# Optimization experiments

Measured on AMD Instinct MI355X. Metric: run time of the kernel, lower is better.

## Reference

```python
import jax, jax.numpy as jnp
import numpy as np

H = 16        # num_attention_heads
DH = 64       # attention_head_dim
D = H * DH    # model dim = 1024
FF = 4 * D    # feed-forward inner dim = 4096
SCALE = DH ** -0.5
EPS = 1e-12


def _ln(x, g, b):
    m = jnp.mean(x, axis=-1, keepdims=True)
    v = jnp.mean((x - m) ** 2, axis=-1, keepdims=True)
    return (x - m) * jax.lax.rsqrt(v + EPS) * g + b


def _attn(x, ctx, Wq, Wk, Wv, Wo, bo, mask):
    # x: [B,S,D] (already pre-normed), ctx: [B,T,D], mask: [B,T] int (1=keep) or None
    B, S, _ = x.shape
    T = ctx.shape[1]
    q = (x @ Wq).reshape(B, S, H, DH)
    k = (ctx @ Wk).reshape(B, T, H, DH)
    v = (ctx @ Wv).reshape(B, T, H, DH)
    scores = jnp.einsum('bqhd,bkhd->bhqk', q, k) * SCALE  # [B,H,S,T]
    if mask is not None:
        scores = jnp.where(mask[:, None, None, :] == 0, -jnp.inf, scores)
    probs = jax.nn.softmax(scores, axis=-1)
    out = jnp.einsum('bhqk,bkhd->bqhd', probs, v).reshape(B, S, D)
    return out @ Wo + bo


def _geglu_ff(x, Wff1, bff1, Wff2, bff2):
    y = x @ Wff1 + bff1                 # [B,S,2*FF]
    h, gate = y[..., :FF], y[..., FF:]
    # GEGLU computes exact (erf) gelu in fp32
    g = jax.nn.gelu(gate.astype(jnp.float32), approximate=False).astype(gate.dtype)
    return (h * g) @ Wff2 + bff2


def setup_inputs() -> dict:
    key = jax.random.key(0)
    ks = jax.random.split(key, 24)
    B, S, T = 4, 1024, 1024
    w = lambda k, shp: jax.random.normal(k, shp, dtype=jnp.float32) * 0.02
    inp = {
        'hidden_states': jax.random.normal(ks[0], (B, S, D), dtype=jnp.float32),
        'context': jax.random.normal(ks[1], (B, T, D), dtype=jnp.float32),
        'encoder_key_padding_mask': jnp.ones((B, T), dtype=jnp.int32),
        'g1': jnp.ones((D,), jnp.float32), 'b1': jnp.zeros((D,), jnp.float32),
        'g2': jnp.ones((D,), jnp.float32), 'b2': jnp.zeros((D,), jnp.float32),
        'g3': jnp.ones((D,), jnp.float32), 'b3': jnp.zeros((D,), jnp.float32),
        'Wq1': w(ks[2], (D, D)), 'Wk1': w(ks[3], (D, D)), 'Wv1': w(ks[4], (D, D)),
        'Wo1': w(ks[5], (D, D)), 'bo1': jnp.zeros((D,), jnp.float32),
        'Wq2': w(ks[6], (D, D)), 'Wk2': w(ks[7], (D, D)), 'Wv2': w(ks[8], (D, D)),
        'Wo2': w(ks[9], (D, D)), 'bo2': jnp.zeros((D,), jnp.float32),
        'Wff1': w(ks[10], (D, 2 * FF)), 'bff1': jnp.zeros((2 * FF,), jnp.float32),
        'Wff2': w(ks[11], (FF, D)), 'bff2': jnp.zeros((D,), jnp.float32),
    }
    return inp


def reference(hidden_states, context, encoder_key_padding_mask,
              g1, b1, g2, b2, g3, b3,
              Wq1, Wk1, Wv1, Wo1, bo1,
              Wq2, Wk2, Wv2, Wo2, bo2,
              Wff1, bff1, Wff2, bff2):
    # Self-attention (attn1): context defaults to (normed) hidden_states, no padding mask
    n1 = _ln(hidden_states, g1, b1)
    h = hidden_states + _attn(n1, n1, Wq1, Wk1, Wv1, Wo1, bo1, None)
    # Cross-attention (attn2) with encoder key padding mask
    n2 = _ln(h, g2, b2)
    h = h + _attn(n2, context, Wq2, Wk2, Wv2, Wo2, bo2, encoder_key_padding_mask)
    # GEGLU feed-forward
    h = h + _geglu_ff(_ln(h, g3, b3), Wff1, bff1, Wff2, bff2)
    return h
```

## Files before the change

### kernel.cpp

```cpp
#include <hip/hip_runtime.h>

typedef unsigned short u16;
typedef unsigned int u32;

#define B_ 4
#define S_ 1024
#define D_ 1024
#define H_ 16
#define DH_ 64
#define FF_ 4096
#define M_ 4096
#define SCALE_ 0.125f

typedef __attribute__((ext_vector_type(8))) __bf16 bf16x8;
typedef __attribute__((ext_vector_type(4))) float f32x4;

__device__ __forceinline__ f32x4 mfma16(bf16x8 a, bf16x8 b, f32x4 c) {
  return __builtin_amdgcn_mfma_f32_16x16x32_bf16(a, b, c, 0, 0, 0);
}

__device__ __forceinline__ u16 f2bf(float x) {
  union { __bf16 h; u16 u; } cv; cv.h = (__bf16)x; return cv.u;
}
__device__ __forceinline__ float bf2f(u16 u) {
  union { u32 u; float f; } cv; cv.u = ((u32)u) << 16; return cv.f;
}
__device__ __forceinline__ u32 packbf2(float a, float b) {
  union { u32 u; __bf16 h[2]; } pk;
  pk.h[0] = (__bf16)a; pk.h[1] = (__bf16)b;
  return pk.u;
}
__device__ __forceinline__ float gelu_exact(float x) {
  return 0.5f * x * (1.f + erff(x * 0.7071067811865475f));
}
__device__ __forceinline__ void gload16(const void* g, void* l) {
  __builtin_amdgcn_global_load_lds((__attribute__((address_space(1))) void*)(g),
                                   (__attribute__((address_space(3))) void*)(l),
                                   16, 0, 0);
}

template<int EPI>
__global__ __launch_bounds__(256, 2) void gemm128(
    const u16* __restrict__ A, const u16* __restrict__ BT,
    const float* __restrict__ bias, const float* __restrict__ res,
    const u16* __restrict__ aux, void* __restrict__ out,
    int M, int N, int K, int ktiles)
{
  __shared__ u16 As[2][128 * 64];
  __shared__ u16 Bs[2][128 * 64];

  const int tid = threadIdx.x;
  const int wave = tid >> 6, lane = tid & 63;
  const int wm = wave >> 1, wn = wave & 1;
  const int qi = lane & 15, g = lane >> 4;

  const int gx = N >> 7;
  const int nwg = gx * (M >> 7);
  int id = blockIdx.y * gridDim.x + blockIdx.x;
  id = (id & 7) * (nwg >> 3) + (id >> 3);
  const int m0 = (id / gx) << 7, n0 = (id % gx) << 7;

  const int NT = ktiles;
  const int kbase = blockIdx.z * ktiles * 64;

  const int r0 = tid >> 3;
  const int scol = (((tid & 7) ^ ((tid >> 3) & 7)) << 3);
  const int swb = wave << 6;

  f32x4 acc[4][4];
#pragma unroll
  for (int i = 0; i < 4; ++i)
#pragma unroll
    for (int j = 0; j < 4; ++j)
      acc[i][j] = (f32x4){0.f, 0.f, 0.f, 0.f};

#define STAGE_A(t, h, b) {                                                  \
    const int tt = (t) >= NT ? (t) - NT : (t);                              \
    _Pragma("unroll")                                                       \
    for (int i = 0; i < 2; ++i) {                                           \
      const int r = (h) * 64 + i * 32 + r0;                                 \
      gload16(A + (size_t)(m0 + r) * K + kbase + tt * 64 + scol,            \
              &As[b][(h) * 4096 + (i * 256 + swb) * 8]);                    \
    } }
#define STAGE_B(t, h, b) {                                                  \
    const int tt = (t) >= NT ? (t) - NT : (t);                              \
    _Pragma("unroll")                                                       \
    for (int i = 0; i < 2; ++i) {                                           \
      const int r = (h) * 64 + i * 32 + r0;                                 \
      gload16(BT + (size_t)(n0 + r) * K + kbase + tt * 64 + scol,           \
              &Bs[b][(h) * 4096 + (i * 256 + swb) * 8]);                    \
    } }

  bf16x8 af[4][2], bfr[4][2];

#define RD_ALL(b)                                                            \
  _Pragma("unroll") for (int mi = 0; mi < 4; ++mi)                           \
  _Pragma("unroll") for (int kk = 0; kk < 2; ++kk) {                         \
    const int row = wm * 64 + mi * 16 + qi;                                  \
    const int cb = ((kk * 64 + (g << 4)) ^ ((qi & 7) << 4));                 \
    af[mi][kk] = *(const bf16x8*)((const char*)&As[b][0] + row * 128 + cb);  \
  }                                                                          \
  _Pragma("unroll") for (int ni = 0; ni < 4; ++ni)                           \
  _Pragma("unroll") for (int kk = 0; kk < 2; ++kk) {                         \
    const int row = wn * 64 + ni * 16 + qi;                                  \
    const int cb = ((kk * 64 + (g << 4)) ^ ((qi & 7) << 4));                 \
    bfr[ni][kk] = *(const bf16x8*)((const char*)&Bs[b][0] + row * 128 + cb); \
  }

#define MFMA_ALL()                                                           \
  _Pragma("unroll") for (int mi = 0; mi < 4; ++mi)                           \
  _Pragma("unroll") for (int ni = 0; ni < 4; ++ni)                           \
  _Pragma("unroll") for (int kk = 0; kk < 2; ++kk)                           \
    acc[mi][ni] = mfma16(af[mi][kk], bfr[ni][kk], acc[mi][ni]);

#define BAR() __builtin_amdgcn_s_barrier()
#define LGKM0() { asm volatile("s_waitcnt lgkmcnt(0)" ::: "memory");         \
                  __builtin_amdgcn_sched_barrier(0); }
#define VM8() asm volatile("s_waitcnt vmcnt(8)" ::: "memory")
#define PRIO(x) __builtin_amdgcn_s_setprio(x)

  STAGE_A(0, 0, 0); STAGE_A(0, 1, 0); STAGE_B(0, 0, 0); STAGE_B(0, 1, 0);
  STAGE_A(1, 0, 1); STAGE_A(1, 1, 1); STAGE_B(1, 0, 1); STAGE_B(1, 1, 1);
  VM8();
  BAR();

  const int NI = NT >> 1;
  for (int it = 0; it < NI; ++it) {
    const int k = it * 2;
    RD_ALL(0);
    PRIO(1); MFMA_ALL(); PRIO(0);
    LGKM0();
    BAR();
    STAGE_A(k + 2, 0, 0); STAGE_A(k + 2, 1, 0);
    STAGE_B(k + 2, 0, 0); STAGE_B(k + 2, 1, 0);
    VM8();
    BAR();
    RD_ALL(1);
    PRIO(1); MFMA_ALL(); PRIO(0);
    LGKM0();
    BAR();
    STAGE_A(k + 3, 0, 1); STAGE_A(k + 3, 1, 1);
    STAGE_B(k + 3, 0, 1); STAGE_B(k + 3, 1, 1);
    VM8();
    BAR();
  }

#pragma unroll
  for (int mi = 0; mi < 4; ++mi) {
#pragma unroll
    for (int ni = 0; ni < 4; ++ni) {
#pragma unroll
      for (int r = 0; r < 4; ++r) {
        const int m = m0 + wm * 64 + mi * 16 + g * 4 + r;
        const int n = n0 + wn * 64 + ni * 16 + qi;
        float v = acc[mi][ni][r];
        if (EPI == 0 || EPI == 5) {
          const int ts = n >> 10, b = m >> 10, s = m & 1023;
          const int hh = (n >> 6) & 15, dh = n & 63;
          if (EPI == 0 && ts == 0) v *= SCALE_;
          ((u16*)out)[(size_t)ts * (B_ * H_ * S_ * DH_) +
                      (((size_t)(b * H_ + hh) * S_) + s) * DH_ + dh] = f2bf(v);
        } else if (EPI == 1) {
          const size_t idx = (size_t)m * N + n;
          ((float*)out)[idx] = res[idx] + v + bias[n];
        } else if (EPI == 2) {
          ((u16*)out)[(size_t)m * N + n] = f2bf(gelu_exact(v + bias[n]));
        } else if (EPI == 3) {
          const size_t idx = (size_t)m * N + n;
          ((u16*)out)[idx] = f2bf((v + bias[n]) * bf2f(aux[idx]));
        } else {
          const size_t idx = (size_t)blockIdx.z * ((size_t)M * N) +
                             (size_t)m * N + n;
          ((u16*)out)[idx] = f2bf(v);
        }
      }
    }
  }
#undef STAGE_A
#undef STAGE_B
#undef RD_ALL
#undef MFMA_ALL
#undef BAR
#undef LGKM0
#undef VM8
#undef PRIO
}

template<bool DOLN, int NS>
__global__ __launch_bounds__(256) void reduce_ln(
    const u16* __restrict__ p, const float* __restrict__ bias,
    const float* __restrict__ res, float* __restrict__ outf,
    const float* __restrict__ gg, const float* __restrict__ bb,
    u16* __restrict__ outn)
{
  __shared__ float red[8];
  const int row = blockIdx.x, tid = threadIdx.x;
  const size_t base = (size_t)row * 1024 + tid * 4;
  const size_t total = (size_t)M_ * 1024;
  float a0 = 0.f, a1 = 0.f, a2 = 0.f, a3 = 0.f;
#pragma unroll
  for (int s = 0; s < NS; ++s) {
    const uint2 u = *(const uint2*)&p[(size_t)s * total + base];
    a0 += bf2f((u16)(u.x & 0xffff));
    a1 += bf2f((u16)(u.x >> 16));
    a2 += bf2f((u16)(u.y & 0xffff));
    a3 += bf2f((u16)(u.y >> 16));
  }
  const float4 b4 = ((const float4*)bias)[tid];
  const float4 r4 = *(const float4*)&res[base];
  float4 o;
  o.x = r4.x + a0 + b4.x;
  o.y = r4.y + a1 + b4.y;
  o.z = r4.z + a2 + b4.z;
  o.w = r4.w + a3 + b4.w;
  *(float4*)&outf[base] = o;

  if (DOLN) {
    float s1 = o.x + o.y + o.z + o.w;
    float s2 = o.x * o.x + o.y * o.y + o.z * o.z + o.w * o.w;
#pragma unroll
    for (int m = 32; m; m >>= 1) {
      s1 += __shfl_xor(s1, m);
      s2 += __shfl_xor(s2, m);
    }
    const int wave = tid >> 6, lane = tid & 63;
    if (lane == 0) { red[wave * 2] = s1; red[wave * 2 + 1] = s2; }
    __syncthreads();
    const float St = red[0] + red[2] + red[4] + red[6];
    const float SQt = red[1] + red[3] + red[5] + red[7];
    const float mean = St * (1.f / 1024.f);
    float var = SQt * (1.f / 1024.f) - mean * mean;
    var = fmaxf(var, 0.f);
    const float rinv = rsqrtf(var + 1e-12f);
    const float4 g4 = ((const float4*)gg)[tid];
    const float4 bb4 = ((const float4*)bb)[tid];
    uint2 w;
    w.x = packbf2((o.x - mean) * rinv * g4.x + bb4.x,
                  (o.y - mean) * rinv * g4.y + bb4.y);
    w.y = packbf2((o.z - mean) * rinv * g4.z + bb4.z,
                  (o.w - mean) * rinv * g4.w + bb4.w);
    ((uint2*)(outn + (size_t)row * 1024))[tid] = w;
  }
}

template<int NS, bool QSC>
__global__ __launch_bounds__(256) void reduce_perm(
    const u16* __restrict__ p, u16* __restrict__ out, int M, int N)
{
  const size_t flat = ((size_t)blockIdx.x * 256 + threadIdx.x) * 4;
  const size_t total = (size_t)M * N;
  float a0 = 0.f, a1 = 0.f, a2 = 0.f, a3 = 0.f;
#pragma unroll
  for (int s = 0; s < NS; ++s) {
    const uint2 u = *(const uint2*)&p[(size_t)s * total + flat];
    a0 += bf2f((u16)(u.x & 0xffff));
    a1 += bf2f((u16)(u.x >> 16));
    a2 += bf2f((u16)(u.y & 0xffff));
    a3 += bf2f((u16)(u.y >> 16));
  }
  if (QSC) { a0 *= SCALE_; a1 *= SCALE_; a2 *= SCALE_; a3 *= SCALE_; }
  const int m = (int)(flat / N), nb = (int)(flat % N);
  const int ts = nb >> 10, hh = (nb >> 6) & 15, dh = nb & 63;
  const int b = m >> 10, sI = m & 1023;
  uint2 w;
  w.x = packbf2(a0, a1);
  w.y = packbf2(a2, a3);
  *(uint2*)&out[(size_t)ts * (B_ * H_ * S_ * DH_) +
                (((size_t)(b * H_ + hh) * S_) + sI) * DH_ + dh] = w;
}

template<bool MASKED>
__global__ __launch_bounds__(256, 4) void attn_kernel(
    const u16* __restrict__ Q, const u16* __restrict__ Kb,
    const u16* __restrict__ VT, const float* __restrict__ bias,
    u16* __restrict__ O, int S, int T)
{
  __shared__ u16 Ks[64 * 72];
  __shared__ u16 VTs[64 * 72];
  __shared__ u16 Ps[4][16 * 72];
  __shared__ float biasS[64];

  const int bh = blockIdx.y;
  const int b = bh >> 4, h = bh & 15;
  const int tid = threadIdx.x;
  const int wave = tid >> 6, lane = tid & 63;
  const int g = lane >> 4, qi = lane & 15;
  const int q0w = blockIdx.x * 64 + wave * 16;

  const u16* Qb = Q + (size_t)bh * S * DH_;
  const u16* Kg = Kb + (size_t)bh * T * DH_;
  const u16* Vg = VT + (size_t)bh * DH_ * T;

  bf16x8 qf[2];
  qf[0] = *(const bf16x8*)&Qb[(q0w + qi) * DH_ + g * 8];
  qf[1] = *(const bf16x8*)&Qb[(q0w + qi) * DH_ + 32 + g * 8];

  f32x4 acc[4];
#pragma unroll
  for (int i = 0; i < 4; ++i) acc[i] = (f32x4){0.f, 0.f, 0.f, 0.f};
  float l_run = 1e-30f;

  u16* Pw = &Ps[wave][0];

  for (int t0 = 0; t0 < T; t0 += 64) {
    __syncthreads();
#pragma unroll
    for (int i = 0; i < 2; ++i) {
      const int flat = i * 256 + tid;
      const int row = flat >> 3, kc = flat & 7;
      *(uint4*)&Ks[row * 72 + kc * 8] = *(const uint4*)&Kg[(size_t)(t0 + row) * DH_ + kc * 8];
      *(uint4*)&VTs[row * 72 + kc * 8] = *(const uint4*)&Vg[(size_t)row * T + t0 + kc * 8];
    }
    if (MASKED && tid < 64) biasS[tid] = bias[b * T + t0 + tid];
    __syncthreads();

    f32x4 sacc[4];
#pragma unroll
    for (int nt = 0; nt < 4; ++nt) sacc[nt] = (f32x4){0.f, 0.f, 0.f, 0.f};
#pragma unroll
    for (int kk = 0; kk < 2; ++kk) {
#pragma unroll
      for (int nt = 0; nt < 4; ++nt) {
        bf16x8 kf = *(const bf16x8*)&Ks[(nt * 16 + qi) * 72 + kk * 32 + g * 8];
        sacc[nt] = mfma16(kf, qf[kk], sacc[nt]);
      }
    }
    float p[4][4];
    float lsum = 0.f;
#pragma unroll
    for (int nt = 0; nt < 4; ++nt)
#pragma unroll
      for (int r = 0; r < 4; ++r) {
        float v = sacc[nt][r];
        if (MASKED) v += biasS[nt * 16 + g * 4 + r];
        const float e = __expf(v);
        p[nt][r] = e;
        lsum += e;
      }
    lsum += __shfl_xor(lsum, 16);
    lsum += __shfl_xor(lsum, 32);
    l_run += lsum;

#pragma unroll
    for (int nt = 0; nt < 4; ++nt) {
      uint2 w;
      w.x = packbf2(p[nt][0], p[nt][1]);
      w.y = packbf2(p[nt][2], p[nt][3]);
      *(uint2*)&Pw[qi * 72 + nt * 16 + g * 4] = w;
    }

#pragma unroll
    for (int kk = 0; kk < 2; ++kk) {
      bf16x8 pf = *(const bf16x8*)&Pw[qi * 72 + kk * 32 + g * 8];
#pragma unroll
      for (int ndh = 0; ndh < 4; ++ndh) {
        bf16x8 vf = *(const bf16x8*)&VTs[(ndh * 16 + qi) * 72 + kk * 32 + g * 8];
        acc[ndh] = mfma16(vf, pf, acc[ndh]);
      }
    }
  }

  const float inv = 1.f / l_run;
  const int qg = q0w + qi;
#pragma unroll
  for (int ndh = 0; ndh < 4; ++ndh) {
    uint2 w;
    w.x = packbf2(acc[ndh][0] * inv, acc[ndh][1] * inv);
    w.y = packbf2(acc[ndh][2] * inv, acc[ndh][3] * inv);
    *(uint2*)&O[(size_t)(b * S_ + qg) * D_ + h * DH_ + ndh * 16 + g * 4] = w;
  }
}

__global__ __launch_bounds__(256) void ln_kernel(
    const float* __restrict__ x, const float* __restrict__ gg,
    const float* __restrict__ bb, u16* __restrict__ out)
{
  __shared__ float red[8];
  const int row = blockIdx.x, tid = threadIdx.x;
  const float4 v = ((const float4*)(x + (size_t)row * D_))[tid];
  float s = v.x + v.y + v.z + v.w;
  float sq = v.x * v.x + v.y * v.y + v.z * v.z + v.w * v.w;
#pragma unroll
  for (int m = 32; m; m >>= 1) {
    s += __shfl_xor(s, m);
    sq += __shfl_xor(sq, m);
  }
  const int wave = tid >> 6, lane = tid & 63;
  if (lane == 0) { red[wave * 2] = s; red[wave * 2 + 1] = sq; }
  __syncthreads();
  const float St = red[0] + red[2] + red[4] + red[6];
  const float SQt = red[1] + red[3] + red[5] + red[7];
  const float mean = St * (1.f / 1024.f);
  float var = SQt * (1.f / 1024.f) - mean * mean;
  var = fmaxf(var, 0.f);
  const float rinv = rsqrtf(var + 1e-12f);
  const float4 g4 = ((const float4*)gg)[tid];
  const float4 b4 = ((const float4*)bb)[tid];
  uint2 o;
  o.x = packbf2((v.x - mean) * rinv * g4.x + b4.x, (v.y - mean) * rinv * g4.y + b4.y);
  o.y = packbf2((v.z - mean) * rinv * g4.z + b4.z, (v.w - mean) * rinv * g4.w + b4.w);
  ((uint2*)(out + (size_t)row * D_))[tid] = o;
}

__global__ __launch_bounds__(256) void transpose_w(
    const float* __restrict__ in, u16* __restrict__ out, int K, int N)
{
  __shared__ float tile[32][33];
  const int tx = threadIdx.x & 31, ty = threadIdx.x >> 5;
  const int k0 = blockIdx.y * 32, n0 = blockIdx.x * 32;
#pragma unroll
  for (int j = 0; j < 4; ++j)
    tile[ty + 8 * j][tx] = in[(size_t)(k0 + ty + 8 * j) * N + n0 + tx];
  __syncthreads();
#pragma unroll
  for (int j = 0; j < 4; ++j)
    out[(size_t)(n0 + ty + 8 * j) * K + k0 + tx] = f2bf(tile[tx][ty + 8 * j]);
}

__global__ __launch_bounds__(256) void transpose_v(
    const u16* __restrict__ in, u16* __restrict__ out, int T)
{
  __shared__ u16 tile[32][33];
  const int tx = threadIdx.x & 31, ty = threadIdx.x >> 5;
  const int bh = blockIdx.z;
  const int t0 = blockIdx.x * 32, d0 = blockIdx.y * 32;
  const u16* ib = in + (size_t)bh * T * DH_;
  u16* ob = out + (size_t)bh * DH_ * T;
#pragma unroll
  for (int j = 0; j < 4; ++j)
    tile[ty + 8 * j][tx] = ib[(size_t)(t0 + ty + 8 * j) * DH_ + d0 + tx];
  __syncthreads();
#pragma unroll
  for (int j = 0; j < 4; ++j)
    ob[(size_t)(d0 + ty + 8 * j) * T + t0 + tx] = tile[tx][ty + 8 * j];
}

__global__ void cvt_bf16(const float* __restrict__ in, u16* __restrict__ out, int n4)
{
  const int i = blockIdx.x * blockDim.x + threadIdx.x;
  if (i < n4) {
    const float4 v = ((const float4*)in)[i];
    uint2 o;
    o.x = packbf2(v.x, v.y);
    o.y = packbf2(v.z, v.w);
    ((uint2*)out)[i] = o;
  }
}

__global__ void mask_bias(const int* __restrict__ mask, float* __restrict__ bias, int n)
{
  const int i = blockIdx.x * blockDim.x + threadIdx.x;
  if (i < n) bias[i] = mask[i] ? 0.f : -1e30f;
}

extern "C" void kernel_launch(void* const* d_in, const int* in_sizes, int n_in,
                              void* d_out, int out_size, void* d_ws, size_t ws_size,
                              hipStream_t stream)
{
  (void)in_sizes; (void)n_in; (void)out_size; (void)ws_size;
  const float* hidden = (const float*)d_in[0];
  const float* ctx    = (const float*)d_in[1];
  const int*   mask   = (const int*)d_in[2];
  const float* g1 = (const float*)d_in[3];
  const float* b1 = (const float*)d_in[4];
  const float* g2 = (const float*)d_in[5];
  const float* b2 = (const float*)d_in[6];
  const float* g3 = (const float*)d_in[7];
  const float* b3 = (const float*)d_in[8];
  const float* Wq1 = (const float*)d_in[9];
  const float* Wk1 = (const float*)d_in[10];
  const float* Wv1 = (const float*)d_in[11];
  const float* Wo1 = (const float*)d_in[12];
  const float* bo1 = (const float*)d_in[13];
  const float* Wq2 = (const float*)d_in[14];
  const float* Wk2 = (const float*)d_in[15];
  const float* Wv2 = (const float*)d_in[16];
  const float* Wo2 = (const float*)d_in[17];
  const float* bo2 = (const float*)d_in[18];
  const float* Wff1 = (const float*)d_in[19];
  const float* bff1 = (const float*)d_in[20];
  const float* Wff2 = (const float*)d_in[21];
  const float* bff2 = (const float*)d_in[22];

  char* ws = (char*)d_ws;
  size_t off = 0;
  auto alloc = [&](size_t bytes) -> void* {
    void* p = ws + off;
    off += (bytes + 255) & ~(size_t)255;
    return p;
  };
  u16* WqT1  = (u16*)alloc((size_t)1024 * 1024 * 2);
  u16* WkT1  = (u16*)alloc((size_t)1024 * 1024 * 2);
  u16* WvT1  = (u16*)alloc((size_t)1024 * 1024 * 2);
  u16* WoT1  = (u16*)alloc((size_t)1024 * 1024 * 2);
  u16* WqT2  = (u16*)alloc((size_t)1024 * 1024 * 2);
  u16* WkT2  = (u16*)alloc((size_t)1024 * 1024 * 2);
  u16* WvT2  = (u16*)alloc((size_t)1024 * 1024 * 2);
  u16* WoT2  = (u16*)alloc((size_t)1024 * 1024 * 2);
  u16* Wff1T = (u16*)alloc((size_t)8192 * 1024 * 2);
  u16* Wff2T = (u16*)alloc((size_t)1024 * 4096 * 2);
  u16* nbuf  = (u16*)alloc((size_t)M_ * D_ * 2);
  u16* hgbuf = (u16*)alloc((size_t)M_ * FF_ * 2);
  u16* qbuf  = (u16*)alloc((size_t)M_ * D_ * 2);
  u16* kbuf  = (u16*)alloc((size_t)M_ * D_ * 2);
  u16* vbuf  = (u16*)alloc((size_t)M_ * D_ * 2);
  u16* vtbuf = (u16*)alloc((size_t)M_ * D_ * 2);
  u16* attnb = (u16*)alloc((size_t)M_ * D_ * 2);
  u16* ctxb  = (u16*)alloc((size_t)M_ * D_ * 2);
  u16* pbuf  = (u16*)alloc((size_t)4 * M_ * D_ * 2);
  float* biasw = (float*)alloc((size_t)B_ * S_ * 4);
  u16* gbuf = qbuf;
  float* hres = (float*)d_out;

  const dim3 blk(256);
  const dim3 gW(32, 32);
  const dim3 gQKV(24, 32);
  const dim3 gKV(16, 32);
  const dim3 gFF(32, 32);
  const dim3 gS2(8, 32, 2);
  const dim3 gF2(8, 32, 4);
  const dim3 gA(16, 64);
  const dim3 gV(32, 2, 64);
  const dim3 gR(4096);

  transpose_w<<<gW, blk, 0, stream>>>(Wq1, WqT1, 1024, 1024);
  transpose_w<<<gW, blk, 0, stream>>>(Wk1, WkT1, 1024, 1024);
  transpose_w<<<gW, blk, 0, stream>>>(Wv1, WvT1, 1024, 1024);
  transpose_w<<<gW, blk, 0, stream>>>(Wo1, WoT1, 1024, 1024);
  transpose_w<<<gW, blk, 0, stream>>>(Wq2, WqT2, 1024, 1024);
  transpose_w<<<gW, blk, 0, stream>>>(Wk2, WkT2, 1024, 1024);
  transpose_w<<<gW, blk, 0, stream>>>(Wv2, WvT2, 1024, 1024);
  transpose_w<<<gW, blk, 0, stream>>>(Wo2, WoT2, 1024, 1024);
  transpose_w<<<dim3(256, 32), blk, 0, stream>>>(Wff1, Wff1T, 1024, 8192);
  transpose_w<<<dim3(32, 128), blk, 0, stream>>>(Wff2, Wff2T, 4096, 1024);
  cvt_bf16<<<dim3((1048576 + 255) / 256), blk, 0, stream>>>(ctx, ctxb, 1048576);
  mask_bias<<<dim3(16), blk, 0, stream>>>(mask, biasw, B_ * S_);

  ln_kernel<<<dim3(M_), blk, 0, stream>>>(hidden, g1, b1, nbuf);
  gemm128<0><<<gQKV, blk, 0, stream>>>(nbuf, WqT1, nullptr, nullptr, nullptr,
                                       qbuf, M_, 3072, 1024, 16);
  transpose_v<<<gV, blk, 0, stream>>>(vbuf, vtbuf, 1024);
  attn_kernel<false><<<gA, blk, 0, stream>>>(qbuf, kbuf, vtbuf, nullptr, attnb, S_, S_);
  gemm128<4><<<gS2, blk, 0, stream>>>(attnb, WoT1, nullptr, nullptr, nullptr,
                                      pbuf, M_, 1024, 1024, 8);
  reduce_ln<true, 2><<<gR, blk, 0, stream>>>(pbuf, bo1, hidden, hres, g2, b2, nbuf);

  gemm128<4><<<gS2, blk, 0, stream>>>(nbuf, WqT2, nullptr, nullptr, nullptr,
                                      pbuf, M_, 1024, 1024, 8);
  reduce_perm<2, true><<<gR, blk, 0, stream>>>(pbuf, qbuf, M_, 1024);
  gemm128<5><<<gKV, blk, 0, stream>>>(ctxb, WkT2, nullptr, nullptr, nullptr,
                                      kbuf, M_, 2048, 1024, 16);
  transpose_v<<<gV, blk, 0, stream>>>(vbuf, vtbuf, 1024);
  attn_kernel<true><<<gA, blk, 0, stream>>>(qbuf, kbuf, vtbuf, biasw, attnb, S_, S_);
  gemm128<4><<<gS2, blk, 0, stream>>>(attnb, WoT2, nullptr, nullptr, nullptr,
                                      pbuf, M_, 1024, 1024, 8);
  reduce_ln<true, 2><<<gR, blk, 0, stream>>>(pbuf, bo2, hres, hres, g3, b3, nbuf);

  gemm128<2><<<gFF, blk, 0, stream>>>(nbuf, Wff1T + (size_t)FF_ * 1024, bff1 + FF_,
                                      nullptr, nullptr, gbuf, M_, FF_, 1024, 16);
  gemm128<3><<<gFF, blk, 0, stream>>>(nbuf, Wff1T, bff1, nullptr, gbuf, hgbuf,
                                      M_, FF_, 1024, 16);
  gemm128<4><<<gF2, blk, 0, stream>>>(hgbuf, Wff2T, nullptr, nullptr, nullptr,
                                      pbuf, M_, 1024, 4096, 16);
  reduce_ln<false, 4><<<gR, blk, 0, stream>>>(pbuf, bff2, hres, hres, nullptr,
                                              nullptr, nullptr);
}
```

Baseline: 418.5 us.

## Replace double-buffered GEMM pipeline with single-buffer loop and 4-way split-K

Removes the two-stage LDS double-buffered GEMM main loop, with its priority hints and manual waitcnt, and replaces it with a simple single-buffer loop: load a tile, sync, compute. This halves LDS use and drops the occupancy hint. Separately, the 1024-K projection GEMMs now use 4-way split-K instead of 2-way, with matching reductions. The simpler loop gives up the overlap between global loads and MFMA, so GEMM throughput is likely to drop, and the extra split-K partials add reduction traffic.

New measurement: 449.9 us. 1.07x slower.

```diff
diff --git a/kernel.cpp b/kernel.cpp
--- a/kernel.cpp
+++ b/kernel.cpp
@@ -40,14 +40,14 @@
 }
 
 template<int EPI>
-__global__ __launch_bounds__(256, 2) void gemm128(
+__global__ __launch_bounds__(256) void gemm128(
     const u16* __restrict__ A, const u16* __restrict__ BT,
     const float* __restrict__ bias, const float* __restrict__ res,
     const u16* __restrict__ aux, void* __restrict__ out,
     int M, int N, int K, int ktiles)
 {
-  __shared__ u16 As[2][128 * 64];
-  __shared__ u16 Bs[2][128 * 64];
+  __shared__ u16 As[128 * 64];
+  __shared__ u16 Bs[128 * 64];
 
   const int tid = threadIdx.x;
   const int wave = tid >> 6, lane = tid & 63;
@@ -74,37 +74,35 @@
     for (int j = 0; j < 4; ++j)
       acc[i][j] = (f32x4){0.f, 0.f, 0.f, 0.f};
 
-#define STAGE_A(t, h, b) {                                                  \
-    const int tt = (t) >= NT ? (t) - NT : (t);                              \
+#define STAGE_A(t, h) {                                                     \
     _Pragma("unroll")                                                       \
     for (int i = 0; i < 2; ++i) {                                           \
       const int r = (h) * 64 + i * 32 + r0;                                 \
-      gload16(A + (size_t)(m0 + r) * K + kbase + tt * 64 + scol,            \
-              &As[b][(h) * 4096 + (i * 256 + swb) * 8]);                    \
+      gload16(A + (size_t)(m0 + r) * K + kbase + (t) * 64 + scol,           \
+              &As[(h) * 4096 + (i * 256 + swb) * 8]);                       \
     } }
-#define STAGE_B(t, h, b) {                                                  \
-    const int tt = (t) >= NT ? (t) - NT : (t);                              \
+#define STAGE_B(t, h) {                                                     \
     _Pragma("unroll")                                                       \
     for (int i = 0; i < 2; ++i) {                                           \
       const int r = (h) * 64 + i * 32 + r0;                                 \
-      gload16(BT + (size_t)(n0 + r) * K + kbase + tt * 64 + scol,           \
-              &Bs[b][(h) * 4096 + (i * 256 + swb) * 8]);                    \
+      gload16(BT + (size_t)(n0 + r) * K + kbase + (t) * 64 + scol,          \
+              &Bs[(h) * 4096 + (i * 256 + swb) * 8]);                       \
     } }
 
   bf16x8 af[4][2], bfr[4][2];
 
-#define RD_ALL(b)                                                            \
+#define RD_ALL()                                                             \
   _Pragma("unroll") for (int mi = 0; mi < 4; ++mi)                           \
   _Pragma("unroll") for (int kk = 0; kk < 2; ++kk) {                         \
     const int row = wm * 64 + mi * 16 + qi;                                  \
     const int cb = ((kk * 64 + (g << 4)) ^ ((qi & 7) << 4));                 \
-    af[mi][kk] = *(const bf16x8*)((const char*)&As[b][0] + row * 128 + cb);  \
+    af[mi][kk] = *(const bf16x8*)((const char*)&As[0] + row * 128 + cb);     \
   }                                                                          \
   _Pragma("unroll") for (int ni = 0; ni < 4; ++ni)                           \
   _Pragma("unroll") for (int kk = 0; kk < 2; ++kk) {                         \
     const int row = wn * 64 + ni * 16 + qi;                                  \
     const int cb = ((kk * 64 + (g << 4)) ^ ((qi & 7) << 4));                 \
-    bfr[ni][kk] = *(const bf16x8*)((const char*)&Bs[b][0] + row * 128 + cb); \
+    bfr[ni][kk] = *(const bf16x8*)((const char*)&Bs[0] + row * 128 + cb);    \
   }
 
 #define MFMA_ALL()                                                           \
@@ -113,36 +111,12 @@
   _Pragma("unroll") for (int kk = 0; kk < 2; ++kk)                           \
     acc[mi][ni] = mfma16(af[mi][kk], bfr[ni][kk], acc[mi][ni]);
 
-#define BAR() __builtin_amdgcn_s_barrier()
-#define LGKM0() { asm volatile("s_waitcnt lgkmcnt(0)" ::: "memory");         \
-                  __builtin_amdgcn_sched_barrier(0); }
-#define VM8() asm volatile("s_waitcnt vmcnt(8)" ::: "memory")
-#define PRIO(x) __builtin_amdgcn_s_setprio(x)
-
-  STAGE_A(0, 0, 0); STAGE_A(0, 1, 0); STAGE_B(0, 0, 0); STAGE_B(0, 1, 0);
-  STAGE_A(1, 0, 1); STAGE_A(1, 1, 1); STAGE_B(1, 0, 1); STAGE_B(1, 1, 1);
-  VM8();
-  BAR();
-
-  const int NI = NT >> 1;
-  for (int it = 0; it < NI; ++it) {
-    const int k = it * 2;
-    RD_ALL(0);
-    PRIO(1); MFMA_ALL(); PRIO(0);
-    LGKM0();
-    BAR();
-    STAGE_A(k + 2, 0, 0); STAGE_A(k + 2, 1, 0);
-    STAGE_B(k + 2, 0, 0); STAGE_B(k + 2, 1, 0);
-    VM8();
-    BAR();
-    RD_ALL(1);
-    PRIO(1); MFMA_ALL(); PRIO(0);
-    LGKM0();
-    BAR();
-    STAGE_A(k + 3, 0, 1); STAGE_A(k + 3, 1, 1);
-    STAGE_B(k + 3, 0, 1); STAGE_B(k + 3, 1, 1);
-    VM8();
-    BAR();
+  for (int t = 0; t < NT; ++t) {
+    if (t) __syncthreads();
+    STAGE_A(t, 0); STAGE_A(t, 1); STAGE_B(t, 0); STAGE_B(t, 1);
+    __syncthreads();
+    RD_ALL();
+    MFMA_ALL();
   }
 
 #pragma unroll
@@ -180,10 +154,6 @@
 #undef STAGE_B
 #undef RD_ALL
 #undef MFMA_ALL
-#undef BAR
-#undef LGKM0
-#undef VM8
-#undef PRIO
 }
 
 template<bool DOLN, int NS>
@@ -517,8 +487,8 @@
   const dim3 gQKV(24, 32);
   const dim3 gKV(16, 32);
   const dim3 gFF(32, 32);
-  const dim3 gS2(8, 32, 2);
-  const dim3 gF2(8, 32, 4);
+  const dim3 gS4(8, 32, 4);
+  const dim3 gF4(8, 32, 4);
   const dim3 gA(16, 64);
   const dim3 gV(32, 2, 64);
   const dim3 gR(4096);
@@ -541,26 +511,26 @@
                                        qbuf, M_, 3072, 1024, 16);
   transpose_v<<<gV, blk, 0, stream>>>(vbuf, vtbuf, 1024);
   attn_kernel<false><<<gA, blk, 0, stream>>>(qbuf, kbuf, vtbuf, nullptr, attnb, S_, S_);
-  gemm128<4><<<gS2, blk, 0, stream>>>(attnb, WoT1, nullptr, nullptr, nullptr,
-                                      pbuf, M_, 1024, 1024, 8);
-  reduce_ln<true, 2><<<gR, blk, 0, stream>>>(pbuf, bo1, hidden, hres, g2, b2, nbuf);
-
-  gemm128<4><<<gS2, blk, 0, stream>>>(nbuf, WqT2, nullptr, nullptr, nullptr,
-                                      pbuf, M_, 1024, 1024, 8);
-  reduce_perm<2, true><<<gR, blk, 0, stream>>>(pbuf, qbuf, M_, 1024);
+  gemm128<4><<<gS4, blk, 0, stream>>>(attnb, WoT1, nullptr, nullptr, nullptr,
+                                      pbuf, M_, 1024, 1024, 4);
+  reduce_ln<true, 4><<<gR, blk, 0, stream>>>(pbuf, bo1, hidden, hres, g2, b2, nbuf);
+
+  gemm128<4><<<gS4, blk, 0, stream>>>(nbuf, WqT2, nullptr, nullptr, nullptr,
+                                      pbuf, M_, 1024, 1024, 4);
+  reduce_perm<4, true><<<gR, blk, 0, stream>>>(pbuf, qbuf, M_, 1024);
   gemm128<5><<<gKV, blk, 0, stream>>>(ctxb, WkT2, nullptr, nullptr, nullptr,
                                       kbuf, M_, 2048, 1024, 16);
   transpose_v<<<gV, blk, 0, stream>>>(vbuf, vtbuf, 1024);
   attn_kernel<true><<<gA, blk, 0, stream>>>(qbuf, kbuf, vtbuf, biasw, attnb, S_, S_);
-  gemm128<4><<<gS2, blk, 0, stream>>>(attnb, WoT2, nullptr, nullptr, nullptr,
-                                      pbuf, M_, 1024, 1024, 8);
-  reduce_ln<true, 2><<<gR, blk, 0, stream>>>(pbuf, bo2, hres, hres, g3, b3, nbuf);
+  gemm128<4><<<gS4, blk, 0, stream>>>(attnb, WoT2, nullptr, nullptr, nullptr,
+                                      pbuf, M_, 1024, 1024, 4);
+  reduce_ln<true, 4><<<gR, blk, 0, stream>>>(pbuf, bo2, hres, hres, g3, b3, nbuf);
 
   gemm128<2><<<gFF, blk, 0, stream>>>(nbuf, Wff1T + (size_t)FF_ * 1024, bff1 + FF_,
                                       nullptr, nullptr, gbuf, M_, FF_, 1024, 16);
   gemm128<3><<<gFF, blk, 0, stream>>>(nbuf, Wff1T, bff1, nullptr, gbuf, hgbuf,
                                       M_, FF_, 1024, 16);
-  gemm128<4><<<gF2, blk, 0, stream>>>(hgbuf, Wff2T, nullptr, nullptr, nullptr,
+  gemm128<4><<<gF4, blk, 0, stream>>>(hgbuf, Wff2T, nullptr, nullptr, nullptr,
                                       pbuf, M_, 1024, 4096, 16);
   reduce_ln<false, 4><<<gR, blk, 0, stream>>>(pbuf, bff2, hres, hres, nullptr,
                                               nullptr, nullptr);
```
